# Performance work log

Measured on AMD Instinct MI355X. Metric: run time of the kernel, lower is better.

The kernel has to match this reference:

```python
import jax, jax.numpy as jnp
import numpy as np

H, L, N = 512, 4096, 64

def make_dplr_hippo(n):
    # HiPPO-LegS -> NPLR -> DPLR diagonalization (numpy, init-time only)
    p0 = np.sqrt(1 + 2 * np.arange(n))
    A = p0[:, None] * p0[None, :]
    A = -(np.tril(A) - np.diag(np.arange(n)))
    p = np.sqrt(np.arange(n) + 0.5)
    b = np.sqrt(2 * np.arange(n) + 1.0)
    S = A + p[:, None] * p[None, :]
    Lambda_re = np.full(n, np.diagonal(S).mean())
    Lambda_im, V = np.linalg.eigh(S * -1j)
    Pc = V.conj().T @ p
    Bc = V.conj().T @ b
    return Lambda_re, Lambda_im, Pc, Bc

def setup_inputs() -> dict:
    key = jax.random.key(0)
    k_u, k_c, k_s = jax.random.split(key, 3)
    lr, li, Pc, Bc = make_dplr_hippo(N)
    tile = lambda v: jnp.tile(jnp.asarray(v, jnp.float32)[None, :], (H, 1))
    dt_min, dt_max = 0.001, 0.1
    log_step = (jax.random.uniform(k_s, (H, 1), jnp.float32)
                * (np.log(dt_max) - np.log(dt_min)) + np.log(dt_min))
    return {
        "u": jax.random.normal(k_u, (H, L), jnp.float32),
        "Lambda_re": tile(lr), "Lambda_im": tile(li),
        "P_re": tile(Pc.real), "P_im": tile(Pc.imag),
        "B_re": tile(Bc.real), "B_im": tile(Bc.imag),
        "C": jax.random.normal(k_c, (H, N, 2), jnp.float32) * (0.5 ** 0.5),
        "D": jnp.ones((H, 1), jnp.float32),
        "log_step": log_step,
    }

def reference(u, Lambda_re, Lambda_im, P_re, P_im, B_re, B_im, C, D, log_step):
    # u: [H, L]; all params leading dim H (vmapped channels)
    Lam = jnp.minimum(Lambda_re, -1e-4) + 1j * Lambda_im      # [H, N]
    P = P_re + 1j * P_im                                       # [H, N]
    B = B_re + 1j * B_im                                       # [H, N]
    Cc = C[..., 0] + 1j * C[..., 1]                             # [H, N]
    step = jnp.exp(log_step)                                    # [H, 1]
    Lseq = u.shape[-1]
    Omega = jnp.exp(-2j * jnp.pi * (jnp.arange(Lseq) / Lseq)).astype(jnp.complex64)  # [L]
    g = (2.0 / step) * ((1.0 - Omega) / (1.0 + Omega))[None, :]  # [H, L]
    c = 2.0 / (1.0 + Omega)                                      # [L]
    denom = 1.0 / (g[:, :, None] - Lam[:, None, :])              # [H, L, N]
    cauchy = lambda v: jnp.einsum('hn,hln->hl', v, denom)
    k00 = cauchy(Cc.conj() * B)
    k01 = cauchy(Cc.conj() * P)
    k10 = cauchy(P.conj() * B)
    k11 = cauchy(P.conj() * P)
    atRoots = c[None, :] * (k00 - k01 * (1.0 / (1.0 + k11)) * k10)
    K = jnp.fft.ifft(atRoots, Lseq, axis=-1).real                # [H, L] conv kernel
    # causal convolution via zero-padded FFT (length 2L)
    ud = jnp.fft.rfft(u, n=2 * Lseq, axis=-1)
    Kd = jnp.fft.rfft(K, n=2 * Lseq, axis=-1)
    y = jnp.fft.irfft(ud * Kd, n=2 * Lseq, axis=-1)[..., :Lseq]
    return y + D * u
```

## Files before the change

### kernel.cpp

```cpp
#include <hip/hip_runtime.h>
#include <math.h>

#define NT 512

typedef float v2 __attribute__((ext_vector_type(2)));

__device__ __forceinline__ v2 vrot(v2 a){ return (v2){-a.y, a.x}; }
__device__ __forceinline__ v2 vconj(v2 a){ return (v2){a.x, -a.y}; }
__device__ __forceinline__ v2 vcmul(v2 a, v2 b){ return a.x*b + a.y*vrot(b); }
__device__ __forceinline__ v2 vfma1(float s, v2 v, v2 acc){
    return (v2){ __builtin_fmaf(s, v.x, acc.x), __builtin_fmaf(s, v.y, acc.y) };
}

__device__ __forceinline__ int SW(int e){ return e ^ (((e>>5) ^ (e>>9)) & 15); }

__device__ __forceinline__ int d4r6(int x){
    int r = (int)(__builtin_bitreverse32((unsigned)x) >> 20);
    return ((r & 0x555) << 1) | ((r >> 1) & 0x555);
}

template<int NB>
__device__ __forceinline__ void r4_dit_inv(v2* buf, int tid, int q) {
    const float fm = 6.2831853072f / (float)(4*q);
    int j0 = tid & (q-1);
    float sb, cb; __sincosf(fm*(float)j0, &sb, &cb);
    v2 W1a = (v2){cb, sb}, W1b = W1a;
    if (q == 1024) { float ss, cs; __sincosf(fm*512.0f, &ss, &cs); W1b = vcmul(W1a, (v2){cs, ss}); }
    v2 W2a = vcmul(W1a,W1a), W3a = vcmul(W2a,W1a);
    v2 W2b = vcmul(W1b,W1b), W3b = vcmul(W2b,W1b);
    #pragma unroll
    for (int i = 0; i < NB; ++i) {
        int b = i*NT + tid;
        int j = b & (q-1);
        int e0 = 4*b - 3*j;
        int a0 = SW(e0), a1 = SW(e0+q), a2 = SW(e0+2*q), a3 = SW(e0+3*q);
        v2 x0 = buf[a0], x1 = buf[a1], x2 = buf[a2], x3 = buf[a3];
        v2 W1 = (i&1)?W1b:W1a, W2 = (i&1)?W2b:W2a, W3 = (i&1)?W3b:W3a;
        v2 t1 = vcmul(x1,W1), t2 = vcmul(x2,W2), t3 = vcmul(x3,W3);
        v2 E0 = x0 + t2, E1 = t1 + t3;
        v2 O0 = x0 - t2, O1 = t1 - t3;
        v2 rO1 = vrot(O1);
        buf[a0] = E0 + E1;
        buf[a2] = E0 - E1;
        buf[a1] = O0 + rO1;
        buf[a3] = O0 - rO1;
    }
    __syncthreads();
}

template<int NB>
__device__ __forceinline__ void r4_dif_fwd(v2* buf, int tid, int q) {
    const float fm = -6.2831853072f / (float)(4*q);
    int j0 = tid & (q-1);
    float sb, cb; __sincosf(fm*(float)j0, &sb, &cb);
    v2 W1a = (v2){cb, sb}, W1b = W1a;
    if (q == 1024) { float ss, cs; __sincosf(fm*512.0f, &ss, &cs); W1b = vcmul(W1a, (v2){cs, ss}); }
    v2 W2a = vcmul(W1a,W1a), W3a = vcmul(W2a,W1a);
    v2 W2b = vcmul(W1b,W1b), W3b = vcmul(W2b,W1b);
    #pragma unroll
    for (int i = 0; i < NB; ++i) {
        int b = i*NT + tid;
        int j = b & (q-1);
        int e0 = 4*b - 3*j;
        int a0 = SW(e0), a1 = SW(e0+q), a2 = SW(e0+2*q), a3 = SW(e0+3*q);
        v2 x0 = buf[a0], x1 = buf[a1], x2 = buf[a2], x3 = buf[a3];
        v2 W1 = (i&1)?W1b:W1a, W2 = (i&1)?W2b:W2a, W3 = (i&1)?W3b:W3a;
        v2 E0 = x0 + x2, E1 = x1 + x3;
        v2 O0 = x0 - x2, O1 = x1 - x3;
        v2 rO1 = vrot(O1);
        buf[a0] = E0 + E1;
        buf[a1] = vcmul(O0 - rO1, W1);
        buf[a2] = vcmul(E0 - E1, W2);
        buf[a3] = vcmul(O0 + rO1, W3);
    }
    __syncthreads();
}

__global__ void __launch_bounds__(NT, 2)
s4_fused(const float* __restrict__ u,
         const float* __restrict__ Lre, const float* __restrict__ Lim,
         const float* __restrict__ Pre, const float* __restrict__ Pim,
         const float* __restrict__ Bre, const float* __restrict__ Bim,
         const float* __restrict__ Cin, const float* __restrict__ Din,
         const float* __restrict__ logstep,
         float* __restrict__ out)
{
    __shared__ v2 buf[8192];
    const int tid = threadIdx.x;
    const int h = blockIdx.x;

    v2* par = buf + 4096;
    if (tid < 64) {
        const int n = tid;
        float lre = fminf(Lre[h*64+n], -1e-4f);
        float lim = Lim[h*64+n];
        par[n] = (v2){lre, lim};
        float pr = Pre[h*64+n], pi = Pim[h*64+n];
        float br = Bre[h*64+n], bi = Bim[h*64+n];
        float cr = Cin[h*128+2*n], ci = Cin[h*128+2*n+1];
        v2 cc = (v2){cr, -ci};
        par[64+n]  = vcmul(cc, (v2){br, bi});
        par[128+n] = vcmul(cc, (v2){pr, pi});
        v2 pc = (v2){pr, -pi};
        par[192+n] = vcmul(pc, (v2){br, bi});
        par[256+n] = (v2){pr*pr + pi*pi, 0.0f};
    }
    __syncthreads();

    const float step = expf(logstep[h]);
    const float tos  = 2.0f / step;

    #pragma unroll 1
    for (int hp = 0; hp < 2; ++hp) {
        v2 g[4], cf[4], k00[4], k01[4], k10[4], k11[4];
        const int lbase = hp*(4*NT);
        #pragma unroll
        for (int i = 0; i < 4; ++i) {
            int l = lbase + i*NT + tid;
            float ang = -6.2831855f * ((float)l * (1.0f/4096.0f));
            double ds, dc;
            sincos((double)ang, &ds, &dc);
            float Omx = (float)dc, Omy = (float)ds;
            float nx = 1.0f-Omx, ny = -Omy;
            float dx = 1.0f+Omx, dy =  Omy;
            float dinv = 1.0f/(dx*dx + dy*dy);
            g[i]  = (v2){tos*((nx*dx+ny*dy)*dinv), tos*((ny*dx-nx*dy)*dinv)};
            cf[i] = (v2){2.0f*dx*dinv, -2.0f*dy*dinv};
            k00[i]=(v2)(0.0f); k01[i]=(v2)(0.0f); k10[i]=(v2)(0.0f); k11[i]=(v2)(0.0f);
        }
        #pragma unroll 1
        for (int n = 0; n < 64; ++n) {
            v2 lam = par[n];
            v2 w00 = par[64+n], w01 = par[128+n], w10 = par[192+n];
            float w11r = par[256+n].x;
            #pragma unroll
            for (int i = 0; i < 4; ++i) {
                v2 d = g[i] - lam;
                float inv = __builtin_amdgcn_rcpf(d.x*d.x + d.y*d.y);
                v2 p  = d * inv;
                v2 cp = (v2){p.x, -p.y};
                v2 rp = (v2){p.y,  p.x};
                k00[i] = vfma1(w00.y, rp, vfma1(w00.x, cp, k00[i]));
                k01[i] = vfma1(w01.y, rp, vfma1(w01.x, cp, k01[i]));
                k10[i] = vfma1(w10.y, rp, vfma1(w10.x, cp, k10[i]));
                k11[i] = vfma1(w11r,  cp, k11[i]);
            }
        }
        #pragma unroll
        for (int i = 0; i < 4; ++i) {
            int l = lbase + i*NT + tid;
            v2 opk = (v2){1.0f + k11[i].x, k11[i].y};
            float iv = 1.0f/(opk.x*opk.x + opk.y*opk.y);
            v2 r11 = vconj(opk) * iv;
            v2 t  = vcmul(vcmul(k01[i], r11), k10[i]);
            buf[SW(d4r6(l))] = vcmul(cf[i], k00[i] - t);
        }
    }
    __syncthreads();

    #pragma unroll 1
    for (int q = 1; q <= 1024; q *= 4) r4_dit_inv<2>(buf, tid, q);

    {
        float kv[8], uval[8];
        #pragma unroll
        for (int i = 0; i < 8; ++i) {
            int l = i*NT + tid;
            kv[i]   = buf[SW(l)].x * (1.0f/4096.0f);
            uval[i] = u[h*4096 + l];
        }
        __syncthreads();
        #pragma unroll
        for (int i = 0; i < 8; ++i) {
            int l = i*NT + tid;
            buf[SW(l)]      = (v2){uval[i], kv[i]};
            buf[SW(l+4096)] = (v2)(0.0f);
        }
    }
    __syncthreads();

    {
        const float fm = -6.2831853072f / 8192.0f;
        float sb, cb; __sincosf(fm*(float)tid, &sb, &cb);
        float ss, cs; __sincosf(fm*512.0f, &ss, &cs);
        v2 cur = (v2){cb, sb};
        const v2 stp = (v2){cs, ss};
        #pragma unroll 1
        for (int i = 0; i < 8; ++i) {
            int j = i*NT + tid;
            int a0 = SW(j), a1 = SW(j+4096);
            v2 a = buf[a0], c = buf[a1];
            buf[a0] = a + c;
            buf[a1] = vcmul(a - c, cur);
            cur = vcmul(cur, stp);
        }
        __syncthreads();
    }
    #pragma unroll 1
    for (int q = 1024; q >= 1; q >>= 2) r4_dif_fwd<4>(buf, tid, q);

    {
        const float fm = 6.2831853072f / 8192.0f;
        v2 v[8];
        #pragma unroll 1
        for (int i = 0; i < 8; ++i) {
            int r  = i*NT + tid;
            float sw_, cw_; __sincosf(fm*(float)r, &sw_, &cw_);
            v2 cur = (v2){cw_, sw_};
            int k1 = r,        k1c = (8192 - r) & 8191;
            int k2 = r + 4096, k2c = 4096 - r;
            v2 za = buf[SW(((k1 &1)<<12) + d4r6(k1 >>1))];
            v2 zb = buf[SW(((k1c&1)<<12) + d4r6(k1c>>1))];
            v2 zc = buf[SW(((k2 &1)<<12) + d4r6(k2 >>1))];
            v2 zd = buf[SW(((k2c&1)<<12) + d4r6(k2c>>1))];
            v2 U1 = 0.5f*(za + vconj(zb));
            v2 K1 = -0.5f*vrot(za - vconj(zb));
            v2 Yr = vcmul(U1, K1);
            v2 U2 = 0.5f*(zc + vconj(zd));
            v2 K2 = -0.5f*vrot(zc - vconj(zd));
            v2 Ys = vcmul(U2, K2);
            v[i] = (Yr + Ys) + vrot(vcmul(cur, Yr - Ys));
        }
        __syncthreads();
        #pragma unroll
        for (int i = 0; i < 8; ++i) {
            int r = i*NT + tid;
            buf[SW(d4r6(r))] = v[i];
        }
        __syncthreads();
    }

    #pragma unroll 1
    for (int q = 1; q <= 1024; q *= 4) r4_dit_inv<2>(buf, tid, q);

    {
        const float Dh = Din[h];
        const float sc = 1.0f / 8192.0f;
        const v2* u2 = (const v2*)(u + h*4096);
        v2*     out2 = (v2*)(out + h*4096);
        #pragma unroll
        for (int i = 0; i < 4; ++i) {
            int n = i*NT + tid;
            v2 p  = buf[SW(n)];
            v2 uu = u2[n];
            out2[n] = sc*p + Dh*uu;
        }
    }
}

extern "C" void kernel_launch(void* const* d_in, const int* in_sizes, int n_in,
                              void* d_out, int out_size, void* d_ws, size_t ws_size,
                              hipStream_t stream)
{
    const float* u       = (const float*)d_in[0];
    const float* Lre     = (const float*)d_in[1];
    const float* Lim     = (const float*)d_in[2];
    const float* Pre     = (const float*)d_in[3];
    const float* Pim     = (const float*)d_in[4];
    const float* Bre     = (const float*)d_in[5];
    const float* Bim     = (const float*)d_in[6];
    const float* Cin     = (const float*)d_in[7];
    const float* Din     = (const float*)d_in[8];
    const float* logstep = (const float*)d_in[9];
    float* out = (float*)d_out;
    const int H = in_sizes[8];
    hipLaunchKernelGGL(s4_fused, dim3(H), dim3(NT), 0, stream,
                       u, Lre, Lim, Pre, Pim, Bre, Bim, Cin, Din, logstep, out);
}
```

Measured before the change: 176.3 us.

## Switch FFTs to radix-8 inverse and fused radix-16 forward passes

Replaces the six-pass radix-4 inverse 4096-point FFTs with four radix-8 passes, and rewrites the 8192-point forward FFT as a fused radix-2×4 first stage, two radix-16 register passes and a final radix-4 pass. Fewer passes mean fewer shared-memory round trips and barriers. The bit-reversal permutation changes from base-4 to base-8 digit reversal. Launch bounds are raised to allow 4 blocks per CU and the Cauchy loop is unrolled by 2, which adds register pressure and may cause spills under the tighter register limit.

```diff
diff --git a/kernel.cpp b/kernel.cpp
--- a/kernel.cpp
+++ b/kernel.cpp
@@ -18,65 +18,60 @@
     int r = (int)(__builtin_bitreverse32((unsigned)x) >> 20);
     return ((r & 0x555) << 1) | ((r >> 1) & 0x555);
 }
-
-template<int NB>
-__device__ __forceinline__ void r4_dit_inv(v2* buf, int tid, int q) {
-    const float fm = 6.2831853072f / (float)(4*q);
-    int j0 = tid & (q-1);
-    float sb, cb; __sincosf(fm*(float)j0, &sb, &cb);
-    v2 W1a = (v2){cb, sb}, W1b = W1a;
-    if (q == 1024) { float ss, cs; __sincosf(fm*512.0f, &ss, &cs); W1b = vcmul(W1a, (v2){cs, ss}); }
-    v2 W2a = vcmul(W1a,W1a), W3a = vcmul(W2a,W1a);
-    v2 W2b = vcmul(W1b,W1b), W3b = vcmul(W2b,W1b);
+__device__ __forceinline__ int d8r4(int x){
+    return ((x&7)<<9) | (((x>>3)&7)<<6) | (((x>>6)&7)<<3) | ((x>>9)&7);
+}
+
+__device__ __forceinline__ void dft8_inv(v2 t[8], v2 y[8]) {
+    const float RH = 0.70710678f;
+    v2 p  = t[0]+t[4], m  = t[0]-t[4], q  = t[2]+t[6], r  = t[2]-t[6];
+    v2 rr = vrot(r);
+    v2 E0 = p+q, E2 = p-q, E1 = m+rr, E3 = m-rr;
+    v2 p2 = t[1]+t[5], m2 = t[1]-t[5], q2 = t[3]+t[7], r2 = t[3]-t[7];
+    v2 rr2 = vrot(r2);
+    v2 O0 = p2+q2, O2 = p2-q2, O1 = m2+rr2, O3 = m2-rr2;
+    v2 W1O = RH*(O1 + vrot(O1));
+    v2 W2O = vrot(O2);
+    v2 W3O = vrot(RH*(O3 + vrot(O3)));
+    y[0] = E0 + O0;  y[4] = E0 - O0;
+    y[1] = E1 + W1O; y[5] = E1 - W1O;
+    y[2] = E2 + W2O; y[6] = E2 - W2O;
+    y[3] = E3 + W3O; y[7] = E3 - W3O;
+}
+
+template<bool TW>
+__device__ __forceinline__ void r8_dit_inv(v2* buf, int tid, int q) {
+    int j = tid & (q-1);
+    int base = 8*tid - 7*j;
+    v2 t[8];
     #pragma unroll
-    for (int i = 0; i < NB; ++i) {
-        int b = i*NT + tid;
-        int j = b & (q-1);
-        int e0 = 4*b - 3*j;
-        int a0 = SW(e0), a1 = SW(e0+q), a2 = SW(e0+2*q), a3 = SW(e0+3*q);
-        v2 x0 = buf[a0], x1 = buf[a1], x2 = buf[a2], x3 = buf[a3];
-        v2 W1 = (i&1)?W1b:W1a, W2 = (i&1)?W2b:W2a, W3 = (i&1)?W3b:W3a;
-        v2 t1 = vcmul(x1,W1), t2 = vcmul(x2,W2), t3 = vcmul(x3,W3);
-        v2 E0 = x0 + t2, E1 = t1 + t3;
-        v2 O0 = x0 - t2, O1 = t1 - t3;
-        v2 rO1 = vrot(O1);
-        buf[a0] = E0 + E1;
-        buf[a2] = E0 - E1;
-        buf[a1] = O0 + rO1;
-        buf[a3] = O0 - rO1;
-    }
+    for (int k = 0; k < 8; ++k) t[k] = buf[SW(base + k*q)];
+    if (TW) {
+        const float fm = 6.2831853072f / (float)(8*q);
+        float sb, cb; __sincosf(fm*(float)j, &sb, &cb);
+        v2 W1 = (v2){cb, sb};
+        v2 W2 = vcmul(W1,W1), W3 = vcmul(W1,W2), W4 = vcmul(W2,W2),
+           W5 = vcmul(W2,W3), W6 = vcmul(W3,W3), W7 = vcmul(W3,W4);
+        t[1]=vcmul(t[1],W1); t[2]=vcmul(t[2],W2); t[3]=vcmul(t[3],W3);
+        t[4]=vcmul(t[4],W4); t[5]=vcmul(t[5],W5); t[6]=vcmul(t[6],W6);
+        t[7]=vcmul(t[7],W7);
+    }
+    v2 y[8];
+    dft8_inv(t, y);
+    #pragma unroll
+    for (int m = 0; m < 8; ++m) buf[SW(base + m*q)] = y[m];
     __syncthreads();
 }
 
-template<int NB>
-__device__ __forceinline__ void r4_dif_fwd(v2* buf, int tid, int q) {
-    const float fm = -6.2831853072f / (float)(4*q);
-    int j0 = tid & (q-1);
-    float sb, cb; __sincosf(fm*(float)j0, &sb, &cb);
-    v2 W1a = (v2){cb, sb}, W1b = W1a;
-    if (q == 1024) { float ss, cs; __sincosf(fm*512.0f, &ss, &cs); W1b = vcmul(W1a, (v2){cs, ss}); }
-    v2 W2a = vcmul(W1a,W1a), W3a = vcmul(W2a,W1a);
-    v2 W2b = vcmul(W1b,W1b), W3b = vcmul(W2b,W1b);
-    #pragma unroll
-    for (int i = 0; i < NB; ++i) {
-        int b = i*NT + tid;
-        int j = b & (q-1);
-        int e0 = 4*b - 3*j;
-        int a0 = SW(e0), a1 = SW(e0+q), a2 = SW(e0+2*q), a3 = SW(e0+3*q);
-        v2 x0 = buf[a0], x1 = buf[a1], x2 = buf[a2], x3 = buf[a3];
-        v2 W1 = (i&1)?W1b:W1a, W2 = (i&1)?W2b:W2a, W3 = (i&1)?W3b:W3a;
-        v2 E0 = x0 + x2, E1 = x1 + x3;
-        v2 O0 = x0 - x2, O1 = x1 - x3;
-        v2 rO1 = vrot(O1);
-        buf[a0] = E0 + E1;
-        buf[a1] = vcmul(O0 - rO1, W1);
-        buf[a2] = vcmul(E0 - E1, W2);
-        buf[a3] = vcmul(O0 + rO1, W3);
-    }
-    __syncthreads();
-}
-
-__global__ void __launch_bounds__(NT, 2)
+__device__ __forceinline__ void r4dif(v2& a0, v2& a1, v2& a2, v2& a3, v2 V1, v2 V2, v2 V3){
+    v2 E0 = a0+a2, E1 = a1+a3, O0 = a0-a2, O1 = a1-a3, rr = vrot(O1);
+    a0 = E0+E1;
+    a1 = vcmul(O0-rr, V1);
+    a2 = vcmul(E0-E1, V2);
+    a3 = vcmul(O0+rr, V3);
+}
+
+__global__ void __launch_bounds__(NT, 4)
 s4_fused(const float* __restrict__ u,
          const float* __restrict__ Lre, const float* __restrict__ Lim,
          const float* __restrict__ Pre, const float* __restrict__ Pim,
@@ -128,7 +123,7 @@
             cf[i] = (v2){2.0f*dx*dinv, -2.0f*dy*dinv};
             k00[i]=(v2)(0.0f); k01[i]=(v2)(0.0f); k10[i]=(v2)(0.0f); k11[i]=(v2)(0.0f);
         }
-        #pragma unroll 1
+        #pragma unroll 2
         for (int n = 0; n < 64; ++n) {
             v2 lam = par[n];
             v2 w00 = par[64+n], w01 = par[128+n], w10 = par[192+n];
@@ -153,13 +148,15 @@
             float iv = 1.0f/(opk.x*opk.x + opk.y*opk.y);
             v2 r11 = vconj(opk) * iv;
             v2 t  = vcmul(vcmul(k01[i], r11), k10[i]);
-            buf[SW(d4r6(l))] = vcmul(cf[i], k00[i] - t);
+            buf[SW(d8r4(l))] = vcmul(cf[i], k00[i] - t);
         }
     }
     __syncthreads();
 
-    #pragma unroll 1
-    for (int q = 1; q <= 1024; q *= 4) r4_dit_inv<2>(buf, tid, q);
+    r8_dit_inv<false>(buf, tid, 1);
+    r8_dit_inv<true >(buf, tid, 8);
+    r8_dit_inv<true >(buf, tid, 64);
+    r8_dit_inv<true >(buf, tid, 512);
 
     {
         float kv[8], uval[8];
@@ -179,25 +176,106 @@
     }
     __syncthreads();
 
+    const float RH = 0.70710678f;
+    const v2 C16 = (v2){0.92387953f, -0.38268343f};
     {
         const float fm = -6.2831853072f / 8192.0f;
         float sb, cb; __sincosf(fm*(float)tid, &sb, &cb);
-        float ss, cs; __sincosf(fm*512.0f, &ss, &cs);
-        v2 cur = (v2){cb, sb};
-        const v2 stp = (v2){cs, ss};
-        #pragma unroll 1
-        for (int i = 0; i < 8; ++i) {
-            int j = i*NT + tid;
-            int a0 = SW(j), a1 = SW(j+4096);
-            v2 a = buf[a0], c = buf[a1];
-            buf[a0] = a + c;
-            buf[a1] = vcmul(a - c, cur);
-            cur = vcmul(cur, stp);
-        }
-        __syncthreads();
-    }
-    #pragma unroll 1
-    for (int q = 1024; q >= 1; q >>= 2) r4_dif_fwd<4>(buf, tid, q);
+        v2 w[2]; w[0] = (v2){cb, sb}; w[1] = vcmul(w[0], C16);
+        #pragma unroll
+        for (int jj = 0; jj < 2; ++jj) {
+            int j = tid + 512*jj;
+            v2 W = w[jj];
+            v2 x[4], y[4];
+            #pragma unroll
+            for (int k = 0; k < 4; ++k) { x[k] = buf[SW(j + 1024*k)]; y[k] = buf[SW(j + 1024*k + 4096)]; }
+            v2 a[4], b[4];
+            #pragma unroll
+            for (int k = 0; k < 4; ++k) { a[k] = x[k] + y[k]; b[k] = vcmul(x[k] - y[k], W); }
+            b[1] = RH*(b[1] - vrot(b[1]));
+            b[2] = (v2){b[2].y, -b[2].x};
+            b[3] = (-RH)*(b[3] + vrot(b[3]));
+            v2 V1 = vcmul(W, W), V2 = vcmul(V1, V1), V3 = vcmul(V1, V2);
+            r4dif(a[0], a[1], a[2], a[3], V1, V2, V3);
+            r4dif(b[0], b[1], b[2], b[3], V1, V2, V3);
+            #pragma unroll
+            for (int m = 0; m < 4; ++m) { buf[SW(j + 1024*m)] = a[m]; buf[SW(j + 1024*m + 4096)] = b[m]; }
+        }
+        __syncthreads();
+    }
+    {
+        int r = tid & 63, beta = tid >> 6;
+        int base = 1024*beta + r;
+        v2 x[16];
+        #pragma unroll
+        for (int m = 0; m < 4; ++m)
+            #pragma unroll
+            for (int s = 0; s < 4; ++s) x[4*m+s] = buf[SW(base + 256*m + 64*s)];
+        const float fm = -6.2831853072f / 1024.0f;
+        float sb, cb; __sincosf(fm*(float)r, &sb, &cb);
+        v2 tau = (v2){cb, sb};
+        v2 T = tau;
+        #pragma unroll
+        for (int s = 0; s < 4; ++s) {
+            v2 T2 = vcmul(T,T), T3 = vcmul(T,T2);
+            r4dif(x[0+s], x[4+s], x[8+s], x[12+s], T, T2, T3);
+            T = vcmul(T, C16);
+        }
+        v2 tt = vcmul(tau,tau);
+        v2 U1 = vcmul(tt,tt);
+        v2 U2 = vcmul(U1,U1), U3 = vcmul(U1,U2);
+        #pragma unroll
+        for (int m = 0; m < 4; ++m)
+            r4dif(x[4*m], x[4*m+1], x[4*m+2], x[4*m+3], U1, U2, U3);
+        #pragma unroll
+        for (int m = 0; m < 4; ++m)
+            #pragma unroll
+            for (int s = 0; s < 4; ++s) buf[SW(base + 256*m + 64*s)] = x[4*m+s];
+        __syncthreads();
+    }
+    {
+        int r = tid & 3, B = tid >> 2;
+        int base = 64*B + r;
+        v2 x[16];
+        #pragma unroll
+        for (int m = 0; m < 4; ++m)
+            #pragma unroll
+            for (int s = 0; s < 4; ++s) x[4*m+s] = buf[SW(base + 16*m + 4*s)];
+        const float fm = -6.2831853072f / 64.0f;
+        float sb, cb; __sincosf(fm*(float)r, &sb, &cb);
+        v2 vv = (v2){cb, sb};
+        v2 T = vv;
+        #pragma unroll
+        for (int s = 0; s < 4; ++s) {
+            v2 T2 = vcmul(T,T), T3 = vcmul(T,T2);
+            r4dif(x[0+s], x[4+s], x[8+s], x[12+s], T, T2, T3);
+            T = vcmul(T, C16);
+        }
+        v2 tt = vcmul(vv,vv);
+        v2 U1 = vcmul(tt,tt);
+        v2 U2 = vcmul(U1,U1), U3 = vcmul(U1,U2);
+        #pragma unroll
+        for (int m = 0; m < 4; ++m)
+            r4dif(x[4*m], x[4*m+1], x[4*m+2], x[4*m+3], U1, U2, U3);
+        #pragma unroll
+        for (int m = 0; m < 4; ++m)
+            #pragma unroll
+            for (int s = 0; s < 4; ++s) buf[SW(base + 16*m + 4*s)] = x[4*m+s];
+        __syncthreads();
+    }
+    {
+        #pragma unroll
+        for (int i = 0; i < 4; ++i) {
+            int e = 4*(tid + 512*i);
+            v2 a0 = buf[SW(e)], a1 = buf[SW(e+1)], a2 = buf[SW(e+2)], a3 = buf[SW(e+3)];
+            v2 E0 = a0+a2, E1 = a1+a3, O0 = a0-a2, O1 = a1-a3, rr = vrot(O1);
+            buf[SW(e)]   = E0+E1;
+            buf[SW(e+1)] = O0-rr;
+            buf[SW(e+2)] = E0-E1;
+            buf[SW(e+3)] = O0+rr;
+        }
+        __syncthreads();
+    }
 
     {
         const float fm = 6.2831853072f / 8192.0f;
@@ -225,13 +303,15 @@
         #pragma unroll
         for (int i = 0; i < 8; ++i) {
             int r = i*NT + tid;
-            buf[SW(d4r6(r))] = v[i];
-        }
-        __syncthreads();
-    }
-
-    #pragma unroll 1
-    for (int q = 1; q <= 1024; q *= 4) r4_dit_inv<2>(buf, tid, q);
+            buf[SW(d8r4(r))] = v[i];
+        }
+        __syncthreads();
+    }
+
+    r8_dit_inv<false>(buf, tid, 1);
+    r8_dit_inv<true >(buf, tid, 8);
+    r8_dit_inv<true >(buf, tid, 64);
+    r8_dit_inv<true >(buf, tid, 512);
 
     {
         const float Dh = Din[h];
```

Result: no change. 178.3 us (+1.1%).
